# Kernel optimization log

Measured on AMD Instinct MI355X. Metric: run time of the kernel, lower is better.

The kernel has to match this reference:

```python
import jax, jax.numpy as jnp
import numpy as np

N_USERS = 100000
N_ITEMS = 100000
N_NODES = N_USERS + N_ITEMS
NNZ = 6400000
DIM = 64
N_HOPS = 3


def setup_inputs() -> dict:
    key = jax.random.key(0)
    k1, k2, k3, k4, k5 = jax.random.split(key, 5)
    user_embed = jax.random.normal(k1, (N_USERS, DIM), dtype=jnp.float32)
    item_embed = jax.random.normal(k2, (N_ITEMS, DIM), dtype=jnp.float32)
    # Normalized-adjacency-style positive values for the sparse matrix.
    edge_vals = jax.random.uniform(k3, (NNZ,), dtype=jnp.float32)
    edge_rows = jax.random.randint(k4, (NNZ,), 0, N_NODES, dtype=jnp.int32)
    edge_cols = jax.random.randint(k5, (NNZ,), 0, N_NODES, dtype=jnp.int32)
    return {
        "user_embed": user_embed,
        "item_embed": item_embed,
        "edge_vals": edge_vals,
        "edge_rows": edge_rows,
        "edge_cols": edge_cols,
    }


def reference(user_embed, item_embed, edge_vals, edge_rows, edge_cols):
    # all_embed: [N_NODES, DIM]
    all_embed = jnp.concatenate([user_embed, item_embed], axis=0)
    agg = all_embed
    embs = [all_embed]
    for _ in range(N_HOPS):
        # SpMM in COO form: out[r] += v * agg[c]  for each edge (r, c, v)
        gathered = edge_vals[:, None] * agg[edge_cols]  # [NNZ, DIM]
        agg = jax.ops.segment_sum(gathered, edge_rows, num_segments=N_NODES)
        embs.append(agg)
    embs = jnp.stack(embs, axis=1)  # [N_NODES, N_HOPS+1, DIM]
    return embs[:N_USERS], embs[N_USERS:]
```

## Files before the change

### kernel.cpp

```cpp
#include <hip/hip_runtime.h>

#define N_USERS 100000
#define N_ITEMS 100000
#define N_NODES (N_USERS + N_ITEMS)
#define NNZ 6400000
#define DIM 64
#define NHOPS 3
#define NODE_STRIDE ((NHOPS + 1) * DIM)

#define BROWS 192
#define NBK 1042
#define PTILE 16384
#define NTILES ((NNZ + PTILE - 1) / PTILE)
#define P2CAP 7000

#define WS_BCNT 0
#define WS_BPTR 1056
#define WS_BCUR 2112
#define WS_RP   3168
#define WS_STG  203264
#define WS_MIRA 13003264
#define WS_MIRB 19403264

__device__ __forceinline__ unsigned short f2bf(float f) {
    unsigned u = __float_as_uint(f);
    u += 0x7fffu + ((u >> 16) & 1u);
    return (unsigned short)(u >> 16);
}
__device__ __forceinline__ float bf2f(unsigned short h) {
    return __uint_as_float((unsigned)h << 16);
}

__global__ void zero_bcnt_kernel(int* __restrict__ bcnt) {
    int i = blockIdx.x * blockDim.x + threadIdx.x;
    if (i < NBK) bcnt[i] = 0;
}

__global__ void bhist_kernel(const int* __restrict__ rows, int* __restrict__ bcnt) {
    __shared__ int h[NBK];
    for (int i = threadIdx.x; i < NBK; i += blockDim.x) h[i] = 0;
    __syncthreads();
    int stride = gridDim.x * blockDim.x;
    for (int i = blockIdx.x * blockDim.x + threadIdx.x; i < NNZ; i += stride)
        atomicAdd(&h[(unsigned)rows[i] / BROWS], 1);
    __syncthreads();
    for (int i = threadIdx.x; i < NBK; i += blockDim.x)
        if (h[i]) atomicAdd(&bcnt[i], h[i]);
}

__global__ void bscan_kernel(const int* __restrict__ bcnt,
                             int* __restrict__ bptr, int* __restrict__ bcur) {
    __shared__ int buf[1024];
    int t = threadIdx.x;
    int a = (2 * t < NBK) ? bcnt[2 * t] : 0;
    int b = (2 * t + 1 < NBK) ? bcnt[2 * t + 1] : 0;
    int s = a + b;
    buf[t] = s;
    __syncthreads();
    for (int off = 1; off < 1024; off <<= 1) {
        int v = (t >= off) ? buf[t - off] : 0;
        __syncthreads();
        buf[t] += v;
        __syncthreads();
    }
    int ex = buf[t] - s;
    if (2 * t < NBK)     { bptr[2 * t] = ex;         bcur[2 * t] = ex; }
    if (2 * t + 1 < NBK) { bptr[2 * t + 1] = ex + a; bcur[2 * t + 1] = ex + a; }
    if (t == 0) bptr[NBK] = NNZ;
}

__global__ void __launch_bounds__(1024) partition_kernel(
        const int* __restrict__ rows, const int* __restrict__ cols,
        const float* __restrict__ vals,
        int* __restrict__ bcur, int2* __restrict__ stg) {
    __shared__ int cur[NBK];
    for (int tile = blockIdx.x; tile < NTILES; tile += gridDim.x) {
        for (int i = threadIdx.x; i < NBK; i += 1024) cur[i] = 0;
        __syncthreads();
        const int base = tile * PTILE;
        const int end  = min(base + PTILE, NNZ);
        for (int e = base + (int)threadIdx.x; e < end; e += 1024)
            atomicAdd(&cur[(unsigned)rows[e] / BROWS], 1);
        __syncthreads();
        for (int i = threadIdx.x; i < NBK; i += 1024) {
            int c = cur[i];
            cur[i] = c ? atomicAdd(&bcur[i], c) : 0;
        }
        __syncthreads();
        for (int e = base + (int)threadIdx.x; e < end; e += 1024) {
            int r = rows[e];
            unsigned b = (unsigned)r / BROWS;
            int rl = r - (int)b * BROWS;
            int pos = atomicAdd(&cur[b], 1);
            int2 v;
            v.x = cols[e] | (rl << 18);
            v.y = __float_as_int(vals[e]);
            stg[pos] = v;
        }
        __syncthreads();
    }
}

__global__ void __launch_bounds__(256) pass2_kernel(
        const int* __restrict__ bptr, int2* __restrict__ stg,
        int* __restrict__ row_ptr) {
    __shared__ int2 sd[P2CAP];
    __shared__ int  lh[BROWS];
    __shared__ int  lc[BROWS];
    int b = blockIdx.x;
    int s = bptr[b], e = bptr[b + 1];
    int cnt = min(e - s, P2CAP);
    for (int i = threadIdx.x; i < cnt; i += 256) sd[i] = stg[s + i];
    int t = threadIdx.x;
    if (t < BROWS) lh[t] = 0;
    __syncthreads();
    for (int i = t; i < cnt; i += 256)
        atomicAdd(&lh[(unsigned)sd[i].x >> 18], 1);
    __syncthreads();
    int own = (t < BROWS) ? lh[t] : 0;
    for (int off = 1; off < BROWS; off <<= 1) {
        int u = (t < BROWS && t >= off) ? lh[t - off] : 0;
        __syncthreads();
        if (t < BROWS) lh[t] += u;
        __syncthreads();
    }
    int rowbase = b * BROWS;
    if (t < BROWS) {
        int ex = lh[t] - own;
        lc[t] = ex;
        if (rowbase + t < N_NODES) row_ptr[rowbase + t] = s + ex;
    }
    if (b == NBK - 1 && t == 0) row_ptr[N_NODES] = NNZ;
    __syncthreads();
    for (int i = t; i < cnt; i += 256) {
        int2 d = sd[i];
        int rl = (unsigned)d.x >> 18;
        int pos = atomicAdd(&lc[rl], 1);
        d.x &= 0x3FFFF;
        stg[s + pos] = d;
    }
}

__global__ void init_hop0_kernel(const float4* __restrict__ ue,
                                 const float4* __restrict__ ie,
                                 float* __restrict__ out,
                                 unsigned short* __restrict__ mirA) {
    int i = blockIdx.x * blockDim.x + threadIdx.x;
    if (i >= N_NODES * 16) return;
    int n = i >> 4, q = i & 15;
    float4 v = (n < N_USERS) ? ue[i] : ie[i - N_USERS * 16];
    ((float4*)(out + (size_t)n * NODE_STRIDE))[q] = v;
    ushort4 h;
    h.x = f2bf(v.x); h.y = f2bf(v.y); h.z = f2bf(v.z); h.w = f2bf(v.w);
    *(ushort4*)(mirA + ((size_t)n << 6) + q * 4) = h;
}

__global__ void spmm_bf_kernel(const int* __restrict__ row_ptr,
                               const int2* __restrict__ csr_pair,
                               const unsigned short* __restrict__ src,
                               unsigned short* __restrict__ dst,
                               float* __restrict__ out, int hop, int write_dst) {
    int wid = (blockIdx.x * blockDim.x + threadIdx.x) >> 6;
    if (wid >= N_NODES) return;
    int lane = threadIdx.x & 63;
    int g = lane >> 4;
    int q = lane & 15;
    int s = row_ptr[wid];
    int e = row_ptr[wid + 1];
    float4 acc = make_float4(0.f, 0.f, 0.f, 0.f);
    int j = s + g;
    for (; j + 4 < e; j += 8) {
        int2 p0 = csr_pair[j];
        int2 p1 = csr_pair[j + 4];
        ushort4 h0 = *(const ushort4*)(src + ((size_t)p0.x << 6) + q * 4);
        ushort4 h1 = *(const ushort4*)(src + ((size_t)p1.x << 6) + q * 4);
        float v0 = __int_as_float(p0.y);
        float v1 = __int_as_float(p1.y);
        acc.x += v0 * bf2f(h0.x); acc.y += v0 * bf2f(h0.y);
        acc.z += v0 * bf2f(h0.z); acc.w += v0 * bf2f(h0.w);
        acc.x += v1 * bf2f(h1.x); acc.y += v1 * bf2f(h1.y);
        acc.z += v1 * bf2f(h1.z); acc.w += v1 * bf2f(h1.w);
    }
    if (j < e) {
        int2 p0 = csr_pair[j];
        ushort4 h0 = *(const ushort4*)(src + ((size_t)p0.x << 6) + q * 4);
        float v0 = __int_as_float(p0.y);
        acc.x += v0 * bf2f(h0.x); acc.y += v0 * bf2f(h0.y);
        acc.z += v0 * bf2f(h0.z); acc.w += v0 * bf2f(h0.w);
    }
    acc.x += __shfl_xor(acc.x, 16); acc.y += __shfl_xor(acc.y, 16);
    acc.z += __shfl_xor(acc.z, 16); acc.w += __shfl_xor(acc.w, 16);
    acc.x += __shfl_xor(acc.x, 32); acc.y += __shfl_xor(acc.y, 32);
    acc.z += __shfl_xor(acc.z, 32); acc.w += __shfl_xor(acc.w, 32);
    if (g == 0) {
        ((float4*)(out + (size_t)wid * NODE_STRIDE + hop * DIM))[q] = acc;
        if (write_dst) {
            ushort4 h;
            h.x = f2bf(acc.x); h.y = f2bf(acc.y); h.z = f2bf(acc.z); h.w = f2bf(acc.w);
            *(ushort4*)(dst + ((size_t)wid << 6) + q * 4) = h;
        }
    }
}

extern "C" void kernel_launch(void* const* d_in, const int* in_sizes, int n_in,
                              void* d_out, int out_size, void* d_ws, size_t ws_size,
                              hipStream_t stream) {
    const float* user_e = (const float*)d_in[0];
    const float* item_e = (const float*)d_in[1];
    const float* vals   = (const float*)d_in[2];
    const int*   rows   = (const int*)d_in[3];
    const int*   cols   = (const int*)d_in[4];
    float* out = (float*)d_out;

    int*  wsi     = (int*)d_ws;
    int*  bcnt    = wsi + WS_BCNT;
    int*  bptr    = wsi + WS_BPTR;
    int*  bcur    = wsi + WS_BCUR;
    int*  row_ptr = wsi + WS_RP;
    int2* stg     = (int2*)(wsi + WS_STG);
    unsigned short* mirA = (unsigned short*)(wsi + WS_MIRA);
    unsigned short* mirB = (unsigned short*)(wsi + WS_MIRB);

    hipLaunchKernelGGL(zero_bcnt_kernel, dim3((NBK + 255) / 256), dim3(256), 0, stream, bcnt);
    hipLaunchKernelGGL(bhist_kernel, dim3(1024), dim3(256), 0, stream, rows, bcnt);
    hipLaunchKernelGGL(bscan_kernel, dim3(1), dim3(1024), 0, stream, bcnt, bptr, bcur);
    hipLaunchKernelGGL(partition_kernel, dim3(256), dim3(1024), 0, stream,
                       rows, cols, vals, bcur, stg);
    hipLaunchKernelGGL(pass2_kernel, dim3(NBK), dim3(256), 0, stream, bptr, stg, row_ptr);
    hipLaunchKernelGGL(init_hop0_kernel, dim3((N_NODES * 16 + 255) / 256), dim3(256), 0, stream,
                       (const float4*)user_e, (const float4*)item_e, out, mirA);

    const dim3 sg((N_NODES * 64 + 255) / 256), sb(256);
    hipLaunchKernelGGL(spmm_bf_kernel, sg, sb, 0, stream, row_ptr, stg, mirA, mirB, out, 1, 1);
    hipLaunchKernelGGL(spmm_bf_kernel, sg, sb, 0, stream, row_ptr, stg, mirB, mirA, out, 2, 1);
    hipLaunchKernelGGL(spmm_bf_kernel, sg, sb, 0, stream, row_ptr, stg, mirA, mirB, out, 3, 0);
}
```

Measured before the change: 666.7 us.

## Stage partition tiles in shared memory and widen SpMM gathers to 16-byte loads

The partition kernel now uses one block per 6144-edge tile. Each block sorts its edges by bucket into shared memory using a local prefix scan, then writes each bucket contiguously to global staging, replacing scattered 8-byte stores with grouped writes. The SpMM kernel now has each lane load 8 bf16 values (16 bytes) per edge and 8 edges are processed in parallel per wavefront, which halves the number of gather instructions per row. The cost is more registers per lane and an extra shuffle stage in the reduction. The partition block also needs about 60KB of shared memory, which limits occupancy.

```diff
diff --git a/kernel.cpp b/kernel.cpp
--- a/kernel.cpp
+++ b/kernel.cpp
@@ -10,8 +10,8 @@
 
 #define BROWS 192
 #define NBK 1042
-#define PTILE 16384
-#define NTILES ((NNZ + PTILE - 1) / PTILE)
+#define PTILE 6144
+#define NTILES 1042
 #define P2CAP 7000
 
 #define WS_BCNT 0
@@ -27,8 +27,11 @@
     u += 0x7fffu + ((u >> 16) & 1u);
     return (unsigned short)(u >> 16);
 }
-__device__ __forceinline__ float bf2f(unsigned short h) {
-    return __uint_as_float((unsigned)h << 16);
+__device__ __forceinline__ float blo(int w) {
+    return __uint_as_float((unsigned)w << 16);
+}
+__device__ __forceinline__ float bhi(int w) {
+    return __uint_as_float((unsigned)w & 0xffff0000u);
 }
 
 __global__ void zero_bcnt_kernel(int* __restrict__ bcnt) {
@@ -69,35 +72,72 @@
     if (t == 0) bptr[NBK] = NNZ;
 }
 
-__global__ void __launch_bounds__(1024) partition_kernel(
+__global__ void __launch_bounds__(256) partition_kernel(
         const int* __restrict__ rows, const int* __restrict__ cols,
         const float* __restrict__ vals,
         int* __restrict__ bcur, int2* __restrict__ stg) {
-    __shared__ int cur[NBK];
-    for (int tile = blockIdx.x; tile < NTILES; tile += gridDim.x) {
-        for (int i = threadIdx.x; i < NBK; i += 1024) cur[i] = 0;
-        __syncthreads();
-        const int base = tile * PTILE;
-        const int end  = min(base + PTILE, NNZ);
-        for (int e = base + (int)threadIdx.x; e < end; e += 1024)
-            atomicAdd(&cur[(unsigned)rows[e] / BROWS], 1);
-        __syncthreads();
-        for (int i = threadIdx.x; i < NBK; i += 1024) {
-            int c = cur[i];
-            cur[i] = c ? atomicAdd(&bcur[i], c) : 0;
+    __shared__ int2 sd2[PTILE];
+    __shared__ int  h[NBK];
+    __shared__ int  lp[NBK];
+    __shared__ int  gb[NBK];
+    __shared__ int  sbuf[256];
+    const int tile = blockIdx.x;
+    const int base = tile * PTILE;
+    const int end  = min(base + PTILE, NNZ);
+    const int t = threadIdx.x;
+    for (int i = t; i < NBK; i += 256) h[i] = 0;
+    __syncthreads();
+    for (int e = base + t; e < end; e += 256)
+        atomicAdd(&h[(unsigned)rows[e] / BROWS], 1);
+    __syncthreads();
+    int cbase = t * 5;
+    int loc[5];
+    int s = 0;
+    #pragma unroll
+    for (int k = 0; k < 5; ++k) {
+        int i = cbase + k;
+        loc[k] = (i < NBK) ? h[i] : 0;
+        s += loc[k];
+    }
+    sbuf[t] = s;
+    __syncthreads();
+    for (int off = 1; off < 256; off <<= 1) {
+        int v = (t >= off) ? sbuf[t - off] : 0;
+        __syncthreads();
+        sbuf[t] += v;
+        __syncthreads();
+    }
+    int run = sbuf[t] - s;
+    #pragma unroll
+    for (int k = 0; k < 5; ++k) {
+        int i = cbase + k;
+        if (i < NBK) {
+            lp[i] = run;
+            if (loc[k]) gb[i] = atomicAdd(&bcur[i], loc[k]);
         }
-        __syncthreads();
-        for (int e = base + (int)threadIdx.x; e < end; e += 1024) {
-            int r = rows[e];
-            unsigned b = (unsigned)r / BROWS;
-            int rl = r - (int)b * BROWS;
-            int pos = atomicAdd(&cur[b], 1);
-            int2 v;
-            v.x = cols[e] | (rl << 18);
-            v.y = __float_as_int(vals[e]);
-            stg[pos] = v;
-        }
-        __syncthreads();
+        run += loc[k];
+    }
+    __syncthreads();
+    for (int i = t; i < NBK; i += 256) h[i] = lp[i];
+    __syncthreads();
+    for (int e = base + t; e < end; e += 256) {
+        int r = rows[e];
+        unsigned b = (unsigned)r / BROWS;
+        int rl = r - (int)b * BROWS;
+        int pos = atomicAdd(&h[b], 1);
+        int2 v;
+        v.x = cols[e] | (rl << 18);
+        v.y = __float_as_int(vals[e]);
+        sd2[pos] = v;
+    }
+    __syncthreads();
+    int wv = t >> 6, lane = t & 63, sg = lane >> 3, l8 = lane & 7;
+    int sub = wv * 8 + sg;
+    for (int b0 = sub; b0 < NBK; b0 += 32) {
+        int lo = lp[b0], hi = h[b0];
+        int gbase = gb[b0];
+        for (int i = l8; i < hi - lo; i += 8)
+            stg[gbase + i] = sd2[lo + i];
     }
 }
 
@@ -108,10 +148,11 @@
     __shared__ int  lh[BROWS];
     __shared__ int  lc[BROWS];
     int b = blockIdx.x;
-    int s = bptr[b], e = bptr[b + 1];
+    int s = bptr[b];
+    int e = bptr[b + 1];
     int cnt = min(e - s, P2CAP);
-    for (int i = threadIdx.x; i < cnt; i += 256) sd[i] = stg[s + i];
     int t = threadIdx.x;
+    for (int i = t; i < cnt; i += 256) sd[i] = stg[s + i];
     if (t < BROWS) lh[t] = 0;
     __syncthreads();
     for (int i = t; i < cnt; i += 256)
@@ -163,41 +204,56 @@
     int wid = (blockIdx.x * blockDim.x + threadIdx.x) >> 6;
     if (wid >= N_NODES) return;
     int lane = threadIdx.x & 63;
-    int g = lane >> 4;
-    int q = lane & 15;
+    int g = lane >> 3;
+    int q = lane & 7;
     int s = row_ptr[wid];
     int e = row_ptr[wid + 1];
-    float4 acc = make_float4(0.f, 0.f, 0.f, 0.f);
+    float acc[8];
+    #pragma unroll
+    for (int k = 0; k < 8; ++k) acc[k] = 0.0f;
     int j = s + g;
-    for (; j + 4 < e; j += 8) {
+    for (; j + 8 < e; j += 16) {
         int2 p0 = csr_pair[j];
-        int2 p1 = csr_pair[j + 4];
-        ushort4 h0 = *(const ushort4*)(src + ((size_t)p0.x << 6) + q * 4);
-        ushort4 h1 = *(const ushort4*)(src + ((size_t)p1.x << 6) + q * 4);
+        int2 p1 = csr_pair[j + 8];
+        int4 w0 = *(const int4*)(src + ((size_t)p0.x << 6) + q * 8);
+        int4 w1 = *(const int4*)(src + ((size_t)p1.x << 6) + q * 8);
         float v0 = __int_as_float(p0.y);
         float v1 = __int_as_float(p1.y);
-        acc.x += v0 * bf2f(h0.x); acc.y += v0 * bf2f(h0.y);
-        acc.z += v0 * bf2f(h0.z); acc.w += v0 * bf2f(h0.w);
-        acc.x += v1 * bf2f(h1.x); acc.y += v1 * bf2f(h1.y);
-        acc.z += v1 * bf2f(h1.z); acc.w += v1 * bf2f(h1.w);
+        acc[0] += v0 * blo(w0.x); acc[1] += v0 * bhi(w0.x);
+        acc[2] += v0 * blo(w0.y); acc[3] += v0 * bhi(w0.y);
+        acc[4] += v0 * blo(w0.z); acc[5] += v0 * bhi(w0.z);
+        acc[6] += v0 * blo(w0.w); acc[7] += v0 * bhi(w0.w);
+        acc[0] += v1 * blo(w1.x); acc[1] += v1 * bhi(w1.x);
+        acc[2] += v1 * blo(w1.y); acc[3] += v1 * bhi(w1.y);
+        acc[4] += v1 * blo(w1.z); acc[5] += v1 * bhi(w1.z);
+        acc[6] += v1 * blo(w1.w); acc[7] += v1 * bhi(w1.w);
     }
     if (j < e) {
         int2 p0 = csr_pair[j];
-        ushort4 h0 = *(const ushort4*)(src + ((size_t)p0.x << 6) + q * 4);
+        int4 w0 = *(const int4*)(src + ((size_t)p0.x << 6) + q * 8);
         float v0 = __int_as_float(p0.y);
-        acc.x += v0 * bf2f(h0.x); acc.y += v0 * bf2f(h0.y);
-        acc.z += v0 * bf2f(h0.z); acc.w += v0 * bf2f(h0.w);
-    }
-    acc.x += __shfl_xor(acc.x, 16); acc.y += __shfl_xor(acc.y, 16);
-    acc.z += __shfl_xor(acc.z, 16); acc.w += __shfl_xor(acc.w, 16);
-    acc.x += __shfl_xor(acc.x, 32); acc.y += __shfl_xor(acc.y, 32);
-    acc.z += __shfl_xor(acc.z, 32); acc.w += __shfl_xor(acc.w, 32);
+        acc[0] += v0 * blo(w0.x); acc[1] += v0 * bhi(w0.x);
+        acc[2] += v0 * blo(w0.y); acc[3] += v0 * bhi(w0.y);
+        acc[4] += v0 * blo(w0.z); acc[5] += v0 * bhi(w0.z);
+        acc[6] += v0 * blo(w0.w); acc[7] += v0 * bhi(w0.w);
+    }
+    #pragma unroll
+    for (int k = 0; k < 8; ++k) {
+        acc[k] += __shfl_xor(acc[k], 8);
+        acc[k] += __shfl_xor(acc[k], 16);
+        acc[k] += __shfl_xor(acc[k], 32);
+    }
     if (g == 0) {
-        ((float4*)(out + (size_t)wid * NODE_STRIDE + hop * DIM))[q] = acc;
+        float* op = out + (size_t)wid * NODE_STRIDE + hop * DIM + q * 8;
+        *(float4*)op       = make_float4(acc[0], acc[1], acc[2], acc[3]);
+        *(float4*)(op + 4) = make_float4(acc[4], acc[5], acc[6], acc[7]);
         if (write_dst) {
-            ushort4 h;
-            h.x = f2bf(acc.x); h.y = f2bf(acc.y); h.z = f2bf(acc.z); h.w = f2bf(acc.w);
-            *(ushort4*)(dst + ((size_t)wid << 6) + q * 4) = h;
+            int4 h;
+            h.x = (int)f2bf(acc[0]) | ((int)f2bf(acc[1]) << 16);
+            h.y = (int)f2bf(acc[2]) | ((int)f2bf(acc[3]) << 16);
+            h.z = (int)f2bf(acc[4]) | ((int)f2bf(acc[5]) << 16);
+            h.w = (int)f2bf(acc[6]) | ((int)f2bf(acc[7]) << 16);
+            *(int4*)(dst + ((size_t)wid << 6) + q * 8) = h;
         }
     }
 }
@@ -224,7 +280,7 @@
     hipLaunchKernelGGL(zero_bcnt_kernel, dim3((NBK + 255) / 256), dim3(256), 0, stream, bcnt);
     hipLaunchKernelGGL(bhist_kernel, dim3(1024), dim3(256), 0, stream, rows, bcnt);
     hipLaunchKernelGGL(bscan_kernel, dim3(1), dim3(1024), 0, stream, bcnt, bptr, bcur);
-    hipLaunchKernelGGL(partition_kernel, dim3(256), dim3(1024), 0, stream,
+    hipLaunchKernelGGL(partition_kernel, dim3(NTILES), dim3(256), 0, stream,
                        rows, cols, vals, bcur, stg);
     hipLaunchKernelGGL(pass2_kernel, dim3(NBK), dim3(256), 0, stream, bptr, stg, row_ptr);
     hipLaunchKernelGGL(init_hop0_kernel, dim3((N_NODES * 16 + 255) / 256), dim3(256), 0, stream,
```

New measurement: 672.0 us. About the same (+0.8%).
